# Kernel tuning notes

Measured on AMD Instinct MI355X. Metric: run time of the kernel, lower is better.

## Reference

```python
import jax, jax.numpy as jnp
import numpy as np
from jax import lax

FC = 8      # heads_count
LN_EPS = 1e-5

def _ln(x, g, b):
    mu = jnp.mean(x, axis=-1, keepdims=True)
    var = jnp.mean((x - mu) ** 2, axis=-1, keepdims=True)
    return (x - mu) / jnp.sqrt(var + LN_EPS) * g + b

def _l2norm(x):
    return x / jnp.maximum(jnp.linalg.norm(x, axis=-1, keepdims=True), 1e-12)

def _gelu(x):
    return jax.nn.gelu(x, approximate=False)

def _resize_bilinear(x, oh, ow):
    # x: [N, C, H, W], align_corners=True bilinear (matches F.interpolate)
    h, w = x.shape[2], x.shape[3]
    ys = jnp.linspace(0.0, h - 1.0, oh)
    xs = jnp.linspace(0.0, w - 1.0, ow)
    y0 = jnp.floor(ys).astype(jnp.int32); y1 = jnp.minimum(y0 + 1, h - 1)
    x0 = jnp.floor(xs).astype(jnp.int32); x1 = jnp.minimum(x0 + 1, w - 1)
    dy = (ys - y0).astype(x.dtype)[None, None, :, None]
    dx = (xs - x0).astype(x.dtype)[None, None, None, :]
    rows = x[:, :, y0, :] * (1 - dy) + x[:, :, y1, :] * dy
    return rows[:, :, :, x0] * (1 - dx) + rows[:, :, :, x1] * dx

def _merge_block(x, center, h, w, p):
    # x: [n,l,c], center: [n,s,c]
    n, l, c = x.shape
    hc, wc = h // 2, w // 2
    xn = x.transpose(0, 2, 1).reshape(n, c, h, w)
    cn = center.transpose(0, 2, 1).reshape(n, c, hc, wc)
    up = _resize_bilinear(cn, h, w)
    y = jnp.concatenate([xn, up], axis=1)            # [n,2c,h,w]
    y = y.transpose(0, 2, 3, 1)                      # NHWC
    y = _gelu(y @ p['mb_l0_w'] + p['mb_l0_b'])
    y = y @ p['mb_l1_w'] + p['mb_l1_b']              # [n,h,w,c]
    y = y.transpose(0, 3, 1, 2)                      # NCHW
    mu = jnp.mean(y, axis=(1, 2, 3), keepdims=True)  # GroupNorm(1, c)
    var = jnp.mean((y - mu) ** 2, axis=(1, 2, 3), keepdims=True)
    y = (y - mu) / jnp.sqrt(var + LN_EPS) * p['mb_gn_g'][None, :, None, None] + p['mb_gn_b'][None, :, None, None]
    down = _resize_bilinear(y, hc, wc)
    new_x = y.reshape(n, c, h * w).transpose(0, 2, 1) + x
    new_c = down.reshape(n, c, hc * wc).transpose(0, 2, 1) + center
    return new_x, new_c

def _global_cluster(x0, center1, p):
    n, l, c = x0.shape
    s = center1.shape[1]
    xp = x0 @ p['gc_p0_w'] + p['gc_p0_b']            # [n,l,hd]
    cp = center1 @ p['gc_p1_w'] + p['gc_p1_b']       # [n,s,2hd]
    hd = xp.shape[-1]
    sc = hd // FC
    m = n * FC
    xp = xp.reshape(n, l, FC, sc).transpose(0, 2, 1, 3).reshape(m, l, sc)
    cp = cp.reshape(n, s, FC, 2 * sc).transpose(0, 2, 1, 3).reshape(m, s, 2 * sc)
    cpt, cval = cp[..., :sc], cp[..., sc:]
    sim = jnp.einsum('mlc,msc->mls', _l2norm(xp), _l2norm(cpt))
    sim = jax.nn.sigmoid(p['gc_alpha'] * sim + p['gc_beta'])
    vals = jnp.max(sim, axis=2)                      # [m,l]
    idx = jnp.argmax(sim, axis=2)                    # [m,l]
    disp = vals[..., None] * jnp.take_along_axis(cval, idx[:, :, None], axis=1)  # [m,l,sc]
    disp = disp.reshape(n, FC, l, sc).transpose(0, 2, 1, 3).reshape(n, l, FC * sc)
    return disp @ p['gc_m_w'] + p['gc_m_b']

def _global_block(x0, center1, h, w, p):
    n, l, c = x0.shape
    new = _global_cluster(x0, center1, p)
    new = _ln(new, p['gb_n0_g'], p['gb_n0_b'])
    y = jnp.concatenate([x0, new], axis=2)           # [n,l,2c]
    y = y.reshape(n, h, w, 2 * c)
    y = _gelu(y @ p['gb_lin_w'] + p['gb_lin_b'])     # [n,h,w,2c]
    y = y.transpose(0, 3, 1, 2)                      # NCHW
    y = lax.conv_general_dilated(y, p['gb_conv_w'], (1, 1), ((1, 1), (1, 1)),
                                 dimension_numbers=('NCHW', 'OIHW', 'NCHW'))
    y = y + p['gb_conv_b'][None, :, None, None]
    y = y.reshape(n, c, h * w).transpose(0, 2, 1)    # [n,l,c]
    return _ln(y, p['gb_n1_g'], p['gb_n1_b']) + x0

def setup_inputs() -> dict:
    key = jax.random.key(0)
    ks = jax.random.split(key, 24)
    N, H, W, C, HD = 8, 52, 52, 256, 256
    L = H * W
    S = (H // 2) * (W // 2)
    f32 = jnp.float32
    def xav(k, shape, fin, fout):
        a = (6.0 / (fin + fout)) ** 0.5
        return jax.random.uniform(k, shape, minval=-a, maxval=a, dtype=f32)
    return {
        'x0_16x': jax.random.normal(ks[0], (N, L, C), f32),
        'x1_16x': jax.random.normal(ks[1], (N, L, C), f32),
        'x0_32x': jax.random.normal(ks[2], (N, S, C), f32),
        'x1_32x': jax.random.normal(ks[3], (N, S, C), f32),
        'size0_16x': 52, 'size1_16x': 52,
        'mb_l0_w': xav(ks[4], (2 * C, 2 * C), 2 * C, 2 * C), 'mb_l0_b': jnp.zeros((2 * C,), f32),
        'mb_l1_w': xav(ks[5], (2 * C, C), 2 * C, C), 'mb_l1_b': jnp.zeros((C,), f32),
        'mb_gn_g': jnp.ones((C,), f32), 'mb_gn_b': jnp.zeros((C,), f32),
        'gc_p0_w': xav(ks[6], (C, HD), C, HD), 'gc_p0_b': jnp.zeros((HD,), f32),
        'gc_p1_w': xav(ks[7], (C, 2 * HD), C, 2 * HD), 'gc_p1_b': jnp.zeros((2 * HD,), f32),
        'gc_m_w': xav(ks[8], (HD, C), HD, C), 'gc_m_b': jnp.zeros((C,), f32),
        'gc_alpha': jnp.ones((1,), f32), 'gc_beta': jnp.zeros((1,), f32),
        'gb_n0_g': jnp.ones((C,), f32), 'gb_n0_b': jnp.zeros((C,), f32),
        'gb_lin_w': xav(ks[9], (2 * C, 2 * C), 2 * C, 2 * C), 'gb_lin_b': jnp.zeros((2 * C,), f32),
        'gb_conv_w': xav(ks[10], (C, 2 * C, 3, 3), 2 * C * 9, C * 9), 'gb_conv_b': jnp.zeros((C,), f32),
        'gb_n1_g': jnp.ones((C,), f32), 'gb_n1_b': jnp.zeros((C,), f32),
    }

def reference(x0_16x, x1_16x, x0_32x, x1_32x, size0_16x, size1_16x,
              mb_l0_w, mb_l0_b, mb_l1_w, mb_l1_b, mb_gn_g, mb_gn_b,
              gc_p0_w, gc_p0_b, gc_p1_w, gc_p1_b, gc_m_w, gc_m_b, gc_alpha, gc_beta,
              gb_n0_g, gb_n0_b, gb_lin_w, gb_lin_b, gb_conv_w, gb_conv_b, gb_n1_g, gb_n1_b):
    p = dict(mb_l0_w=mb_l0_w, mb_l0_b=mb_l0_b, mb_l1_w=mb_l1_w, mb_l1_b=mb_l1_b,
             mb_gn_g=mb_gn_g, mb_gn_b=mb_gn_b,
             gc_p0_w=gc_p0_w, gc_p0_b=gc_p0_b, gc_p1_w=gc_p1_w, gc_p1_b=gc_p1_b,
             gc_m_w=gc_m_w, gc_m_b=gc_m_b, gc_alpha=gc_alpha, gc_beta=gc_beta,
             gb_n0_g=gb_n0_g, gb_n0_b=gb_n0_b, gb_lin_w=gb_lin_w, gb_lin_b=gb_lin_b,
             gb_conv_w=gb_conv_w, gb_conv_b=gb_conv_b, gb_n1_g=gb_n1_g, gb_n1_b=gb_n1_b)
    h0 = w0 = int(size0_16x)
    h1 = w1 = int(size1_16x)
    # single layer, type == 'cross' (types=["cross"]); shared weights across streams
    x0_16x, x0_32x = _merge_block(x0_16x, x0_32x, h0, w0, p)
    x1_16x, x1_32x = _merge_block(x1_16x, x1_32x, h1, w1, p)
    x0_16x = _global_block(x0_16x, x1_32x, h0, w0, p)
    x1_16x = _global_block(x1_16x, x0_32x, h1, w1, p)
    return (x0_16x, x1_16x)
```

## Files before the change

### kernel.cpp

```cpp
#include <hip/hip_runtime.h>
#include <math.h>

#define NB 8
#define HH 52
#define WW 52
#define LL 2704
#define CC 256
#define HC 26
#define WC 26
#define SS 676
#define C2 512
#define FCn 8
#define SCn 32
#define M16 (NB*LL)
#define M32 (NB*SS)
#define KCONV (9*C2)
#define SAMP16 ((size_t)LL*CC)
#define SAMP32 ((size_t)SS*CC)

typedef double dvec4 __attribute__((ext_vector_type(4)));
typedef float  f32x4 __attribute__((ext_vector_type(4)));
typedef short  b16x8 __attribute__((ext_vector_type(8)));

__device__ __forceinline__ float  gelu_ct(float x){ return 0.5f*x*(1.0f + erff(x*0.70710678118654752f)); }
__device__ __forceinline__ double gelu_ct(double x){ return 0.5*x*(1.0 + erf(x*0.70710678118654752440)); }

__device__ __forceinline__ short f2b(float x){
    union { float f; unsigned u; } v; v.f = x;
    unsigned r = v.u + 0x7fffu + ((v.u >> 16) & 1u);
    return (short)(r >> 16);
}

template<typename TA0, typename TA1, typename TO, bool GELU, bool CAT>
__global__ __launch_bounds__(256) void gemm_d64(
    const TA0* __restrict__ A0, const TA1* __restrict__ A1, int K0,
    const float* __restrict__ W, const float* __restrict__ Bias,
    TO* __restrict__ Out, int M, int K, int N)
{
    __shared__ double As[16][65];
    __shared__ double Bs[16][65];
    const int t = threadIdx.x;
    const int mBase = blockIdx.y * 64;
    const int nBase = blockIdx.x * 64;
    const int arow = t >> 2;
    const int kof  = (t & 3) << 2;
    const int brow = t >> 4;
    const int nof  = (t & 15) << 2;
    const int w  = t >> 6;
    const int wr = (w >> 1) * 32;
    const int wc = (w & 1) * 32;
    const int lane = t & 63;
    const int lr = lane & 15, lk = lane >> 4;

    dvec4 prm = {0.,0.,0.,0.}, prn = {0.,0.,0.,0.};
    prm = __builtin_amdgcn_mfma_f64_16x16x4f64((double)lr, 0.25, prm, 0,0,0);
    prn = __builtin_amdgcn_mfma_f64_16x16x4f64(0.25, (double)lr, prn, 0,0,0);
    int pm[4], pn[4];
    #pragma unroll
    for (int i=0;i<4;i++){ pm[i] = (int)prm[i]; pn[i] = (int)prn[i]; }

    dvec4 acc00 = {0.,0.,0.,0.}, acc01 = {0.,0.,0.,0.};
    dvec4 acc10 = {0.,0.,0.,0.}, acc11 = {0.,0.,0.,0.};
    const int am = mBase + arow;
    for (int k0 = 0; k0 < K; k0 += 16){
        double a[4] = {0.,0.,0.,0.};
        if (am < M){
            #pragma unroll
            for (int j=0;j<4;j++){
                int k = k0 + kof + j;
                if (!CAT || k < K0) a[j] = (double)A0[(size_t)am*K0 + k];
                else                a[j] = (double)A1[(size_t)am*(K-K0) + (k-K0)];
            }
        }
        double b[4];
        #pragma unroll
        for (int j=0;j<4;j++)
            b[j] = (double)W[(size_t)(k0+brow)*N + nBase + nof + j];
        __syncthreads();
        #pragma unroll
        for (int j=0;j<4;j++) As[kof+j][arow] = a[j];
        #pragma unroll
        for (int j=0;j<4;j++) Bs[brow][nof+j] = b[j];
        __syncthreads();
        #pragma unroll
        for (int ks = 0; ks < 4; ks++){
            double a0 = As[ks*4+lk][wr+lr];
            double a1 = As[ks*4+lk][wr+16+lr];
            double b0 = Bs[ks*4+lk][wc+lr];
            double b1 = Bs[ks*4+lk][wc+16+lr];
            acc00 = __builtin_amdgcn_mfma_f64_16x16x4f64(a0,b0,acc00,0,0,0);
            acc01 = __builtin_amdgcn_mfma_f64_16x16x4f64(a0,b1,acc01,0,0,0);
            acc10 = __builtin_amdgcn_mfma_f64_16x16x4f64(a1,b0,acc10,0,0,0);
            acc11 = __builtin_amdgcn_mfma_f64_16x16x4f64(a1,b1,acc11,0,0,0);
        }
    }
    #pragma unroll
    for (int i=0;i<4;i++){
        const int gm0 = mBase + wr + pm[i];
        const int gm1 = gm0 + 16;
        const int gn0 = nBase + wc + pn[i];
        const int gn1 = gn0 + 16;
        const double bias0 = (double)Bias[gn0];
        const double bias1 = (double)Bias[gn1];
        if (gm0 < M){
            double v0 = acc00[i] + bias0; if (GELU) v0 = gelu_ct(v0);
            double v1 = acc01[i] + bias1; if (GELU) v1 = gelu_ct(v1);
            Out[(size_t)gm0*N + gn0] = (TO)v0;
            Out[(size_t)gm0*N + gn1] = (TO)v1;
        }
        if (gm1 < M){
            double v0 = acc10[i] + bias0; if (GELU) v0 = gelu_ct(v0);
            double v1 = acc11[i] + bias1; if (GELU) v1 = gelu_ct(v1);
            Out[(size_t)gm1*N + gn0] = (TO)v0;
            Out[(size_t)gm1*N + gn1] = (TO)v1;
        }
    }
}

template<bool GELU, bool CAT, bool OUT_BF>
__global__ __launch_bounds__(256) void gemm_bf(
    const short* __restrict__ A0, const short* __restrict__ A1, int K0,
    const short* __restrict__ Wb, const float* __restrict__ Bias,
    void* __restrict__ OutV, int M, int K, int N)
{
    __shared__ short As[64][72];
    __shared__ short Bs[64][72];
    const int t = threadIdx.x;
    const int mBase = blockIdx.y*64, nBase = blockIdx.x*64;
    const int lane = t & 63, lr = lane & 15, lg = lane >> 4;
    const int wr = (t >> 6) * 16;
    const int srow = t >> 2;
    const int sk   = (t & 3) * 16;
    const int am = mBase + srow;
    const int bo = nBase + srow;
    f32x4 acc[4] = {{0,0,0,0},{0,0,0,0},{0,0,0,0},{0,0,0,0}};

    for (int c0 = 0; c0 < K; c0 += 64){
        const int kk = c0 + sk;
        const short* ap;
        if (!CAT || kk < K0) ap = A0 + (size_t)am*K0 + kk;
        else                 ap = A1 + (size_t)am*(K-K0) + (kk - K0);
        b16x8 a0 = *(const b16x8*)ap;
        b16x8 a1 = *(const b16x8*)(ap + 8);
        b16x8 bv0 = *(const b16x8*)&Wb[(size_t)bo*K + kk];
        b16x8 bv1 = *(const b16x8*)&Wb[(size_t)bo*K + kk + 8];
        __syncthreads();
        *(b16x8*)&As[srow][sk]     = a0;
        *(b16x8*)&As[srow][sk + 8] = a1;
        *(b16x8*)&Bs[srow][sk]     = bv0;
        *(b16x8*)&Bs[srow][sk + 8] = bv1;
        __syncthreads();
        #pragma unroll
        for (int kc=0;kc<2;kc++){
            b16x8 a = *(const b16x8*)&As[wr + lr][kc*32 + lg*8];
            #pragma unroll
            for (int cb=0;cb<4;cb++){
                b16x8 b = *(const b16x8*)&Bs[cb*16 + lr][kc*32 + lg*8];
                acc[cb] = __builtin_amdgcn_mfma_f32_16x16x32_bf16(a, b, acc[cb], 0,0,0);
            }
        }
    }
    #pragma unroll
    for (int cb=0;cb<4;cb++){
        int col = nBase + cb*16 + lr;
        float bias = Bias[col];
        #pragma unroll
        for (int i=0;i<4;i++){
            int row = mBase + wr + lg*4 + i;
            float v = acc[cb][i] + bias;
            if (GELU) v = gelu_ct(v);
            if (OUT_BF) ((short*)OutV)[(size_t)row*N + col] = f2b(v);
            else        ((float*)OutV)[(size_t)row*N + col] = v;
        }
    }
}

__global__ __launch_bounds__(256) void conv_bf2(const short* __restrict__ Xb,
    const short* __restrict__ WTb, const float* __restrict__ Bias, float* __restrict__ Out)
{
    __shared__ short As[64][72];
    __shared__ short Bs[256][72];
    const int t = threadIdx.x;
    const int mBase = blockIdx.x*64;
    const int lane = t & 63, lr = lane & 15, lg = lane >> 4;
    const int wr = (t >> 6) * 16;
    const int srow = t >> 2;
    const int sk   = (t & 3) * 16;
    const int am = mBase + srow;
    const int an = am / LL; const int ahw = am % LL;
    const int ah = ahw / WW; const int aw = ahw % WW;
    f32x4 acc[16];
    #pragma unroll
    for (int i=0;i<16;i++) acc[i] = (f32x4){0.f,0.f,0.f,0.f};
    const b16x8 z = {0,0,0,0,0,0,0,0};

    for (int pos = 0; pos < 9; pos++){
        const int dh = pos/3 - 1, dw = pos%3 - 1;
        const int h2 = ah + dh, w2 = aw + dw;
        const bool ok = (h2 >= 0 && h2 < HH && w2 >= 0 && w2 < WW);
        const short* xrow = Xb + ((size_t)(an*LL + h2*WW + w2))*C2;
        for (int c0 = 0; c0 < C2; c0 += 64){
            b16x8 a0 = ok ? *(const b16x8*)&xrow[c0 + sk]     : z;
            b16x8 a1 = ok ? *(const b16x8*)&xrow[c0 + sk + 8] : z;
            b16x8 w0[4], w1[4];
            #pragma unroll
            for (int r=0;r<4;r++){
                const short* wp = WTb + (size_t)(srow + 64*r)*KCONV + pos*C2 + c0 + sk;
                w0[r] = *(const b16x8*)wp;
                w1[r] = *(const b16x8*)(wp + 8);
            }
            __syncthreads();
            *(b16x8*)&As[srow][sk]     = a0;
            *(b16x8*)&As[srow][sk + 8] = a1;
            #pragma unroll
            for (int r=0;r<4;r++){
                *(b16x8*)&Bs[srow + 64*r][sk]     = w0[r];
                *(b16x8*)&Bs[srow + 64*r][sk + 8] = w1[r];
            }
            __syncthreads();
            #pragma unroll
            for (int kc=0;kc<2;kc++){
                b16x8 a = *(const b16x8*)&As[wr + lr][kc*32 + lg*8];
                #pragma unroll
                for (int cb=0;cb<16;cb++){
                    b16x8 b = *(const b16x8*)&Bs[cb*16 + lr][kc*32 + lg*8];
                    acc[cb] = __builtin_amdgcn_mfma_f32_16x16x32_bf16(a, b, acc[cb], 0,0,0);
                }
            }
        }
    }
    #pragma unroll
    for (int cb=0;cb<16;cb++){
        int col = cb*16 + lr;
        float bias = Bias[col];
        #pragma unroll
        for (int i=0;i<4;i++){
            int row = mBase + wr + lg*4 + i;
            Out[(size_t)row*CC + col] = acc[cb][i] + bias;
        }
    }
}

__global__ void wtransb_k(const float* __restrict__ wsrc, short* __restrict__ wt){
    int o = blockIdx.x;
    int i = threadIdx.x;
    #pragma unroll
    for (int pos = 0; pos < 9; pos++)
        wt[(size_t)o*KCONV + pos*C2 + i] = f2b(wsrc[((size_t)o*C2 + i)*9 + pos]);
}

__global__ void wtb_k(const float* __restrict__ src, short* __restrict__ dst, int K, int N){
    int n = blockIdx.x;
    for (int k = threadIdx.x; k < K; k += 256)
        dst[(size_t)n*K + k] = f2b(src[(size_t)k*N + n]);
}

__global__ void d2b_k(const double* __restrict__ src, short* __restrict__ dst){
    int i = blockIdx.x*256 + threadIdx.x;
    dst[i] = f2b((float)src[i]);
}

__global__ void ups_k(const float* __restrict__ cen, double* __restrict__ up){
    int idx = blockIdx.x*256 + threadIdx.x;
    int c = idx & 255;
    int gl = idx >> 8;
    int n = gl / LL, l = gl % LL;
    int h = l / WW, w = l % WW;
    double fy = (h==HH-1) ? (double)(HC-1) : h*((double)(HC-1)/(HH-1));
    double fx = (w==WW-1) ? (double)(WC-1) : w*((double)(WC-1)/(WW-1));
    int y0 = (int)fy; int y1 = min(y0+1, HC-1);
    int x0 = (int)fx; int x1 = min(x0+1, WC-1);
    double dy = fy - y0, dx = fx - x0;
    const float* base = cen + (size_t)n*SAMP32 + c;
    double v00 = (double)base[(size_t)(y0*WC + x0)*CC];
    double v01 = (double)base[(size_t)(y0*WC + x1)*CC];
    double v10 = (double)base[(size_t)(y1*WC + x0)*CC];
    double v11 = (double)base[(size_t)(y1*WC + x1)*CC];
    double r0 = v00*(1.0-dy) + v10*dy;
    double r1 = v01*(1.0-dy) + v11*dy;
    up[idx] = r0*(1.0-dx) + r1*dx;
}

__global__ __launch_bounds__(256) void gn_stats_k(const double* __restrict__ t2c,
    double* __restrict__ stats, int nOff){
    const double* p = t2c + (size_t)blockIdx.y*SAMP16;
    int i0 = blockIdx.x*4096 + threadIdx.x;
    double s = 0.0, q = 0.0;
    #pragma unroll
    for (int r = 0; r < 16; r++){
        double v = p[i0 + r*256];
        s += v; q += v*v;
    }
    #pragma unroll
    for (int off = 32; off; off >>= 1){
        s += __shfl_xor(s, off);
        q += __shfl_xor(q, off);
    }
    __shared__ double ls[4], lq[4];
    int wid = threadIdx.x >> 6;
    if ((threadIdx.x & 63) == 0){ ls[wid] = s; lq[wid] = q; }
    __syncthreads();
    if (threadIdx.x == 0){
        int n = nOff + blockIdx.y;
        atomicAdd(&stats[n*2+0], ls[0]+ls[1]+ls[2]+ls[3]);
        atomicAdd(&stats[n*2+1], lq[0]+lq[1]+lq[2]+lq[3]);
    }
}

__global__ void merge_x_k(const double* __restrict__ t2c, const float* __restrict__ x,
    const float* __restrict__ g, const float* __restrict__ b,
    const double* __restrict__ stats, int nOff, double* __restrict__ mxn){
    int idx = blockIdx.x*256 + threadIdx.x;
    const double inv = 1.0/((double)LL*CC);
    int c = idx & (CC-1);
    int n = nOff + idx / (LL*CC);
    double mu = stats[2*n]*inv;
    double var = stats[2*n+1]*inv - mu*mu;
    double r = 1.0/sqrt(var + 1e-5);
    mxn[idx] = (t2c[idx]-mu)*r*(double)g[c] + (double)b[c] + (double)x[idx];
}

__global__ void merge_c_k(const double* __restrict__ t2c, const float* __restrict__ cen,
    const float* __restrict__ g, const float* __restrict__ b,
    const double* __restrict__ stats, int nOff, double* __restrict__ mcn){
    int idx = blockIdx.x*256 + threadIdx.x;
    int c = idx & 255;
    int ns = idx >> 8;
    int nl = ns / SS, s = ns % SS;
    int i = s / WC, j = s % WC;
    double fy = (i==WC-1) ? (double)(HH-1) : i*((double)(HH-1)/(HC-1));
    double fx = (j==WC-1) ? (double)(WW-1) : j*((double)(WW-1)/(WC-1));
    int y0 = (int)fy; int y1 = min(y0+1, HH-1);
    int x0 = (int)fx; int x1 = min(x0+1, WW-1);
    double dy = fy - y0, dx = fx - x0;
    const double* base = t2c + (size_t)nl*SAMP16 + c;
    double v00 = base[(size_t)(y0*WW + x0)*CC];
    double v01 = base[(size_t)(y0*WW + x1)*CC];
    double v10 = base[(size_t)(y1*WW + x0)*CC];
    double v11 = base[(size_t)(y1*WW + x1)*CC];
    double r0 = v00*(1.0-dy) + v10*dy;
    double r1 = v01*(1.0-dy) + v11*dy;
    double v = r0*(1.0-dx) + r1*dx;
    const double inv = 1.0/((double)LL*CC);
    int n = nOff + nl;
    double mu = stats[2*n]*inv;
    double var = stats[2*n+1]*inv - mu*mu;
    double r = 1.0/sqrt(var + 1e-5);
    mcn[idx] = (v-mu)*r*(double)g[c] + (double)b[c] + (double)cen[idx];
}

__global__ __launch_bounds__(256) void cptn_k(const double* __restrict__ cp, double* __restrict__ ctn){
    int ns = blockIdx.x;
    int n = ns / SS, s = ns % SS;
    int hgrp = threadIdx.x >> 5, k = threadIdx.x & 31;
    double v = cp[(size_t)ns*C2 + hgrp*64 + k];
    double q = v*v;
    #pragma unroll
    for (int off = 16; off; off >>= 1) q += __shfl_xor(q, off, 32);
    double d = fmax(sqrt(q), 1e-12);
    ctn[((size_t)(n*FCn + hgrp)*SS + s)*SCn + k] = v/d;
}

__global__ __launch_bounds__(256) void xnorm_k(const double* __restrict__ xpc, double* __restrict__ xn){
    int t = threadIdx.x;
    int g = t >> 5, k = t & 31;
    int gl = blockIdx.x*8 + g;
    int nl = gl / LL, l = gl % LL;
    int h = blockIdx.y;
    double v = xpc[(size_t)gl*CC + h*SCn + k];
    double q = v*v;
    #pragma unroll
    for (int off = 16; off; off >>= 1) q += __shfl_xor(q, off, 32);
    xn[((size_t)(nl*FCn + h)*LL + l)*SCn + k] = v / fmax(sqrt(q), 1e-12);
}

__global__ __launch_bounds__(256) void sim3_k(
    const double* __restrict__ xn,
    const double* __restrict__ ctn,
    const double* __restrict__ cp,
    const float* __restrict__ alpha_p, const float* __restrict__ beta_p,
    int nOff, short* __restrict__ dispb)
{
    __shared__ double xs[32][65];
    __shared__ double cs[32][65];
    const int t = threadIdx.x;
    const int lBase = blockIdx.x * 64;
    const int h = blockIdx.y;
    const int nl = blockIdx.z;
    const int n = nOff + nl;
    const int w  = t >> 6;
    const int wr = (w >> 1) * 32;
    const int wc = (w & 1) * 32;
    const int lane = t & 63;
    const int lr = lane & 15, lk = lane >> 4;
    const double alpha = (double)alpha_p[0], beta = (double)beta_p[0];

    dvec4 prm = {0.,0.,0.,0.}, prn = {0.,0.,0.,0.};
    prm = __builtin_amdgcn_mfma_f64_16x16x4f64((double)lr, 0.25, prm, 0,0,0);
    prn = __builtin_amdgcn_mfma_f64_16x16x4f64(0.25, (double)lr, prn, 0,0,0);
    int pm[4], pn[4];
    #pragma unroll
    for (int i=0;i<4;i++){ pm[i] = (int)prm[i]; pn[i] = (int)prn[i]; }

    const double* xb = xn + ((size_t)(nl*FCn + h)*LL + lBase)*SCn;
    const int lav = min(64, LL - lBase);
    #pragma unroll
    for (int r = 0; r < 8; r++){
        int idx = t + r*256;
        int li = idx >> 5, ki = idx & 31;
        xs[ki][li] = (li < lav) ? xb[idx] : 0.0;
    }

    double bz[2][2][4];
    int    bs[2][2][4];
    #pragma unroll
    for (int rf=0; rf<2; rf++)
        #pragma unroll
        for (int j=0; j<2; j++)
            #pragma unroll
            for (int i=0; i<4; i++){ bz[rf][j][i] = -1.0e300; bs[rf][j][i] = 0; }

    const double* cbase = ctn + ((size_t)(n*FCn + h))*SS*SCn;
    for (int sBase = 0; sBase < SS; sBase += 64){
        const int sav = min(64, SS - sBase);
        const double* cb = cbase + (size_t)sBase*SCn;
        __syncthreads();
        #pragma unroll
        for (int r = 0; r < 8; r++){
            int idx = t + r*256;
            int si = idx >> 5, ki = idx & 31;
            cs[ki][si] = (si < sav) ? cb[idx] : 0.0;
        }
        __syncthreads();
        dvec4 a00 = {0.,0.,0.,0.}, a01 = {0.,0.,0.,0.};
        dvec4 a10 = {0.,0.,0.,0.}, a11 = {0.,0.,0.,0.};
        #pragma unroll
        for (int ks = 0; ks < 8; ks++){
            double xa0 = xs[ks*4+lk][wr+lr];
            double xa1 = xs[ks*4+lk][wr+16+lr];
            double cb0 = cs[ks*4+lk][wc+lr];
            double cb1 = cs[ks*4+lk][wc+16+lr];
            a00 = __builtin_amdgcn_mfma_f64_16x16x4f64(xa0,cb0,a00,0,0,0);
            a01 = __builtin_amdgcn_mfma_f64_16x16x4f64(xa0,cb1,a01,0,0,0);
            a10 = __builtin_amdgcn_mfma_f64_16x16x4f64(xa1,cb0,a10,0,0,0);
            a11 = __builtin_amdgcn_mfma_f64_16x16x4f64(xa1,cb1,a11,0,0,0);
        }
        #pragma unroll
        for (int i=0;i<4;i++){
            int s0 = sBase + wc + pn[i];
            int s1 = s0 + 16;
            if (s0 < SS){
                double z = alpha*a00[i] + beta;
                if (z > bz[0][0][i]){ bz[0][0][i] = z; bs[0][0][i] = s0; }
                z = alpha*a10[i] + beta;
                if (z > bz[1][0][i]){ bz[1][0][i] = z; bs[1][0][i] = s0; }
            }
            if (s1 < SS){
                double z = alpha*a01[i] + beta;
                if (z > bz[0][1][i]){ bz[0][1][i] = z; bs[0][1][i] = s1; }
                z = alpha*a11[i] + beta;
                if (z > bz[1][1][i]){ bz[1][1][i] = z; bs[1][1][i] = s1; }
            }
        }
    }
    __syncthreads();
    double* redv = &xs[0][0];
    int*    redi = (int*)&cs[0][0];
    #pragma unroll
    for (int rf=0; rf<2; rf++){
        #pragma unroll
        for (int i=0;i<4;i++){
            double z0 = bz[rf][0][i]; int i0 = bs[rf][0][i];
            double z1 = bz[rf][1][i]; int i1 = bs[rf][1][i];
            bool take1 = (z1 > z0) || (z1 == z0 && i1 < i0);
            double z = take1 ? z1 : z0;
            int    s = take1 ? i1 : i0;
            int row = wr + rf*16 + pm[i];
            int cls = (w & 1)*16 + pn[i];
            redv[row*32 + cls] = z;
            redi[row*32 + cls] = s;
        }
    }
    __syncthreads();
    if (t < 64){
        double best = redv[t*32]; int bi = redi[t*32];
        #pragma unroll
        for (int c = 1; c < 32; c++){
            double v = redv[t*32 + c]; int ii = redi[t*32 + c];
            if (v > best || (v == best && ii < bi)){ best = v; bi = ii; }
        }
        int l = lBase + t;
        if (l < LL){
            double val;
            if (best >= 0.0) val = 1.0/(1.0 + exp(-best));
            else { double e = exp(best); val = e/(1.0+e); }
            const double* cv = cp + ((size_t)(n*SS + bi))*C2 + h*64 + 32;
            short* dr = dispb + ((size_t)(n*LL + l))*CC + h*SCn;
            #pragma unroll
            for (int k=0;k<32;k++) dr[k] = f2b((float)(val*cv[k]));
        }
    }
}

__global__ __launch_bounds__(256) void ln_bf_k(const float* __restrict__ y,
    const float* __restrict__ g, const float* __restrict__ b, short* __restrict__ ob){
    int row = blockIdx.x*4 + (threadIdx.x >> 6);
    int lane = threadIdx.x & 63;
    const float* rp = y + (size_t)row*CC;
    float4 v = *(const float4*)(rp + lane*4);
    float s = v.x+v.y+v.z+v.w;
    float q = v.x*v.x+v.y*v.y+v.z*v.z+v.w*v.w;
    #pragma unroll
    for (int off = 32; off; off >>= 1){ s += __shfl_xor(s, off); q += __shfl_xor(q, off); }
    float mu = s*(1.0f/CC);
    float var = q*(1.0f/CC) - mu*mu;
    float r = rsqrtf(var + 1e-5f);
    int c = lane*4;
    float4 gv = *(const float4*)(g+c);
    float4 bv = *(const float4*)(b+c);
    short* op = ob + (size_t)row*CC + c;
    op[0] = f2b((v.x-mu)*r*gv.x+bv.x);
    op[1] = f2b((v.y-mu)*r*gv.y+bv.y);
    op[2] = f2b((v.z-mu)*r*gv.z+bv.z);
    op[3] = f2b((v.w-mu)*r*gv.w+bv.w);
}

__global__ __launch_bounds__(256) void final_k(float* __restrict__ y, const double* __restrict__ res,
    const float* __restrict__ g, const float* __restrict__ b){
    int row = blockIdx.x*4 + (threadIdx.x >> 6);
    int lane = threadIdx.x & 63;
    float* rp = y + (size_t)row*CC;
    const double* xp = res + (size_t)row*CC;
    float4 v = *(const float4*)(rp + lane*4);
    float s = v.x+v.y+v.z+v.w;
    float q = v.x*v.x+v.y*v.y+v.z*v.z+v.w*v.w;
    #pragma unroll
    for (int off = 32; off; off >>= 1){ s += __shfl_xor(s, off); q += __shfl_xor(q, off); }
    float mu = s*(1.0f/CC);
    float var = q*(1.0f/CC) - mu*mu;
    float r = rsqrtf(var + 1e-5f);
    int c = lane*4;
    float4 gv = *(const float4*)(g+c);
    float4 bv = *(const float4*)(b+c);
    float4 o;
    o.x = (v.x-mu)*r*gv.x+bv.x + (float)xp[c+0];
    o.y = (v.y-mu)*r*gv.y+bv.y + (float)xp[c+1];
    o.z = (v.z-mu)*r*gv.z+bv.z + (float)xp[c+2];
    o.w = (v.w-mu)*r*gv.w+bv.w + (float)xp[c+3];
    *(float4*)(rp+c) = o;
}

extern "C" void kernel_launch(void* const* d_in, const int* in_sizes, int n_in,
                              void* d_out, int out_size, void* d_ws, size_t ws_size,
                              hipStream_t stream)
{
    const float* x16[2] = {(const float*)d_in[0], (const float*)d_in[1]};
    const float* x32[2] = {(const float*)d_in[2], (const float*)d_in[3]};
    const float* mb_l0_w = (const float*)d_in[6];
    const float* mb_l0_b = (const float*)d_in[7];
    const float* mb_l1_w = (const float*)d_in[8];
    const float* mb_l1_b = (const float*)d_in[9];
    const float* mb_gn_g = (const float*)d_in[10];
    const float* mb_gn_b = (const float*)d_in[11];
    const float* gc_p0_w = (const float*)d_in[12];
    const float* gc_p0_b = (const float*)d_in[13];
    const float* gc_p1_w = (const float*)d_in[14];
    const float* gc_p1_b = (const float*)d_in[15];
    const float* gc_m_w  = (const float*)d_in[16];
    const float* gc_m_b  = (const float*)d_in[17];
    const float* gc_alpha= (const float*)d_in[18];
    const float* gc_beta = (const float*)d_in[19];
    const float* gb_n0_g = (const float*)d_in[20];
    const float* gb_n0_b = (const float*)d_in[21];
    const float* gb_lin_w= (const float*)d_in[22];
    const float* gb_lin_b= (const float*)d_in[23];
    const float* gb_conv_w=(const float*)d_in[24];
    const float* gb_conv_b=(const float*)d_in[25];
    const float* gb_n1_g = (const float*)d_in[26];
    const float* gb_n1_b = (const float*)d_in[27];

    const size_t F8  = (size_t)M16*CC*8;
    const size_t G8  = (size_t)M32*CC*8;
    const size_t WT4 = (size_t)KCONV*CC*4;

    char* base = (char*)d_ws;
    double* mx[2] = { (double*)base, (double*)(base + F8) };
    double* mc[2] = { (double*)(base + 2*F8), (double*)(base + 2*F8 + G8) };
    char*   pWT   = base + 2*F8 + 2*G8;
    short*  WTb   = (short*)pWT;
    short*  WLb   = (short*)(pWT + 2359296);
    short*  WMb   = (short*)(pWT + 2883584);
    double* stats = (double*)(pWT + WT4);
    char*   E     = pWT + WT4 + 256;
    const size_t base_need = 2*F8 + 2*G8 + WT4 + 256;

    const size_t T2  = (size_t)LL*CC*8;
    const size_t T1  = (size_t)LL*C2*8;
    int nb = 1;
    {
        const int cands[4] = {8,4,2,1};
        for (int ci = 0; ci < 4; ci++){
            int c = cands[ci];
            size_t merge_r  = (size_t)c*(2*T2 + T1);
            size_t global_r = 22151168ull + 11075584ull + (size_t)c*2*T2 + 11075584ull + 11075584ull;
            size_t r = merge_r > global_r ? merge_r : global_r;
            if (base_need + r <= ws_size){ nb = c; break; }
            if (c == 1) return;
        }
    }

    double* t2c = (double*)E;
    double* t1c = (double*)(E + nb*T2);
    double* upc = (double*)(E + nb*(T2 + T1));
    double* cp    = (double*)E;
    double* ctn   = (double*)(E + 22151168);
    double* xpc   = (double*)(E + 33226752);
    double* xn    = (double*)(E + 33226752 + nb*T2);
    short*  dispb = (short*) (E + 33226752 + 2*(size_t)nb*T2);
    short*  mxb   = (short*) (E + 33226752 + 2*(size_t)nb*T2 + 11075584);
    float*  Dbuf  = (float*) E;
    short*  Dbufb = (short*) (E + 22151168);
    short*  Bbufb = (short*) E;

    wtransb_k<<<CC, C2, 0, stream>>>(gb_conv_w, WTb);
    wtb_k<<<C2, 256, 0, stream>>>(gb_lin_w, WLb, C2, C2);
    wtb_k<<<CC, 256, 0, stream>>>(gc_m_w, WMb, CC, CC);

    const int Mc = nb*LL;
    const int mTiles = (Mc + 63) / 64;

    for (int i = 0; i < 2; i++){
        hipMemsetAsync(stats, 0, 16*sizeof(double), stream);
        for (int ch = 0; ch < NB; ch += nb){
            const float* x16c = x16[i] + (size_t)ch*SAMP16;
            const float* x32c = x32[i] + (size_t)ch*SAMP32;
            ups_k<<<nb*LL, 256, 0, stream>>>(x32c, upc);
            gemm_d64<float,double,double,true,true><<<dim3(8, mTiles), 256, 0, stream>>>(
                x16c, upc, CC, mb_l0_w, mb_l0_b, t1c, Mc, C2, C2);
            gemm_d64<double,double,double,false,false><<<dim3(4, mTiles), 256, 0, stream>>>(
                t1c, (const double*)nullptr, C2, mb_l1_w, mb_l1_b, t2c, Mc, C2, CC);
            gn_stats_k<<<dim3(169, nb), 256, 0, stream>>>(t2c, stats, ch);
            merge_x_k<<<nb*LL, 256, 0, stream>>>(t2c, x16c,
                mb_gn_g, mb_gn_b, stats, ch, mx[i] + (size_t)ch*SAMP16);
            merge_c_k<<<nb*SS, 256, 0, stream>>>(t2c, x32c,
                mb_gn_g, mb_gn_b, stats, ch, mc[i] + (size_t)ch*SAMP32);
        }
    }

    float* outp[2] = { (float*)d_out, (float*)d_out + (size_t)M16*CC };
    for (int i = 0; i < 2; i++){
        const double* xi64 = mx[i];
        const double* ci64 = mc[1-i];
        gemm_d64<double,double,double,false,false><<<dim3(8, 85), 256, 0, stream>>>(
            ci64, (const double*)nullptr, CC, gc_p1_w, gc_p1_b, cp, M32, CC, C2);
        cptn_k<<<M32, 256, 0, stream>>>(cp, ctn);
        for (int ch = 0; ch < NB; ch += nb){
            gemm_d64<double,double,double,false,false><<<dim3(4, mTiles), 256, 0, stream>>>(
                xi64 + (size_t)ch*SAMP16, (const double*)nullptr, CC, gc_p0_w, gc_p0_b,
                xpc, Mc, CC, CC);
            xnorm_k<<<dim3(nb*(LL/8), FCn), 256, 0, stream>>>(xpc, xn);
            sim3_k<<<dim3((LL+63)/64, FCn, nb), 256, 0, stream>>>(
                xn, ctn, cp, gc_alpha, gc_beta, ch, dispb);
        }
        d2b_k<<<(M16*CC)/256, 256, 0, stream>>>(xi64, mxb);
        gemm_bf<false,false,false><<<dim3(4, 338), 256, 0, stream>>>(
            dispb, (const short*)nullptr, CC, WMb, gc_m_b, Dbuf, M16, CC, CC);
        ln_bf_k<<<M16/4, 256, 0, stream>>>(Dbuf, gb_n0_g, gb_n0_b, Dbufb);
        gemm_bf<true,true,true><<<dim3(8, 338), 256, 0, stream>>>(
            mxb, Dbufb, CC, WLb, gb_lin_b, Bbufb, M16, C2, C2);
        conv_bf2<<<338, 256, 0, stream>>>(Bbufb, WTb, gb_conv_b, outp[i]);
        final_k<<<M16/4, 256, 0, stream>>>(outp[i], xi64, gb_n1_g, gb_n1_b);
    }
}
```

Measured before the change: 2.570 ms.

## Prefetch fp64 GEMM tiles, shrink conv tile, defer L2 normalization into sim kernel

```diff
diff --git a/kernel.cpp b/kernel.cpp
--- a/kernel.cpp
+++ b/kernel.cpp
@@ -37,14 +37,14 @@
     const float* __restrict__ W, const float* __restrict__ Bias,
     TO* __restrict__ Out, int M, int K, int N)
 {
-    __shared__ double As[16][65];
-    __shared__ double Bs[16][65];
+    __shared__ double As[32][65];
+    __shared__ double Bs[32][65];
     const int t = threadIdx.x;
     const int mBase = blockIdx.y * 64;
     const int nBase = blockIdx.x * 64;
     const int arow = t >> 2;
-    const int kof  = (t & 3) << 2;
-    const int brow = t >> 4;
+    const int kofA = (t & 3) << 3;
+    const int kb   = (t >> 4) << 1;
     const int nof  = (t & 15) << 2;
     const int w  = t >> 6;
     const int wr = (w >> 1) * 32;
@@ -62,28 +62,40 @@
     dvec4 acc00 = {0.,0.,0.,0.}, acc01 = {0.,0.,0.,0.};
     dvec4 acc10 = {0.,0.,0.,0.}, acc11 = {0.,0.,0.,0.};
     const int am = mBase + arow;
-    for (int k0 = 0; k0 < K; k0 += 16){
-        double a[4] = {0.,0.,0.,0.};
-        if (am < M){
-            #pragma unroll
-            for (int j=0;j<4;j++){
-                int k = k0 + kof + j;
-                if (!CAT || k < K0) a[j] = (double)A0[(size_t)am*K0 + k];
-                else                a[j] = (double)A1[(size_t)am*(K-K0) + (k-K0)];
+
+    double aReg[8], bReg[8];
+    auto loadA = [&](int k0){
+        #pragma unroll
+        for (int j=0;j<8;j++){
+            int k = k0 + kofA + j;
+            double v = 0.0;
+            if (am < M){
+                if (!CAT || k < K0) v = (double)A0[(size_t)am*K0 + k];
+                else                v = (double)A1[(size_t)am*(K-K0) + (k-K0)];
             }
-        }
-        double b[4];
-        #pragma unroll
-        for (int j=0;j<4;j++)
-            b[j] = (double)W[(size_t)(k0+brow)*N + nBase + nof + j];
+            aReg[j] = v;
+        }
+    };
+    auto loadB = [&](int k0){
+        #pragma unroll
+        for (int r=0;r<2;r++)
+            #pragma unroll
+            for (int j=0;j<4;j++)
+                bReg[r*4+j] = (double)W[(size_t)(k0+kb+r)*N + nBase + nof + j];
+    };
+    loadA(0); loadB(0);
+    for (int k0 = 0; k0 < K; k0 += 32){
         __syncthreads();
         #pragma unroll
-        for (int j=0;j<4;j++) As[kof+j][arow] = a[j];
-        #pragma unroll
-        for (int j=0;j<4;j++) Bs[brow][nof+j] = b[j];
+        for (int j=0;j<8;j++) As[kofA+j][arow] = aReg[j];
+        #pragma unroll
+        for (int r=0;r<2;r++)
+            #pragma unroll
+            for (int j=0;j<4;j++) Bs[kb+r][nof+j] = bReg[r*4+j];
         __syncthreads();
-        #pragma unroll
-        for (int ks = 0; ks < 4; ks++){
+        if (k0 + 32 < K){ loadA(k0+32); loadB(k0+32); }
+        #pragma unroll
+        for (int ks = 0; ks < 8; ks++){
             double a0 = As[ks*4+lk][wr+lr];
             double a1 = As[ks*4+lk][wr+16+lr];
             double b0 = Bs[ks*4+lk][wc+lr];
@@ -178,20 +190,24 @@
 __global__ __launch_bounds__(256) void conv_bf2(const short* __restrict__ Xb,
     const short* __restrict__ WTb, const float* __restrict__ Bias, float* __restrict__ Out)
 {
-    __shared__ short As[64][72];
+    __shared__ short As[32][72];
     __shared__ short Bs[256][72];
     const int t = threadIdx.x;
-    const int mBase = blockIdx.x*64;
+    const int mBase = blockIdx.x*32;
     const int lane = t & 63, lr = lane & 15, lg = lane >> 4;
-    const int wr = (t >> 6) * 16;
+    const int w = t >> 6;
+    const int wr16 = (w & 1) * 16;
+    const int ch   = (w >> 1) * 8;
+    const int arow = t >> 3;
+    const int ska  = (t & 7) * 8;
     const int srow = t >> 2;
     const int sk   = (t & 3) * 16;
-    const int am = mBase + srow;
+    const int am = mBase + arow;
     const int an = am / LL; const int ahw = am % LL;
     const int ah = ahw / WW; const int aw = ahw % WW;
-    f32x4 acc[16];
-    #pragma unroll
-    for (int i=0;i<16;i++) acc[i] = (f32x4){0.f,0.f,0.f,0.f};
+    f32x4 acc[8];
+    #pragma unroll
+    for (int i=0;i<8;i++) acc[i] = (f32x4){0.f,0.f,0.f,0.f};
     const b16x8 z = {0,0,0,0,0,0,0,0};
 
     for (int pos = 0; pos < 9; pos++){
@@ -200,8 +216,7 @@
         const bool ok = (h2 >= 0 && h2 < HH && w2 >= 0 && w2 < WW);
         const short* xrow = Xb + ((size_t)(an*LL + h2*WW + w2))*C2;
         for (int c0 = 0; c0 < C2; c0 += 64){
-            b16x8 a0 = ok ? *(const b16x8*)&xrow[c0 + sk]     : z;
-            b16x8 a1 = ok ? *(const b16x8*)&xrow[c0 + sk + 8] : z;
+            b16x8 a0 = ok ? *(const b16x8*)&xrow[c0 + ska] : z;
             b16x8 w0[4], w1[4];
             #pragma unroll
             for (int r=0;r<4;r++){
@@ -210,8 +225,7 @@
                 w1[r] = *(const b16x8*)(wp + 8);
             }
             __syncthreads();
-            *(b16x8*)&As[srow][sk]     = a0;
-            *(b16x8*)&As[srow][sk + 8] = a1;
+            *(b16x8*)&As[arow][ska] = a0;
             #pragma unroll
             for (int r=0;r<4;r++){
                 *(b16x8*)&Bs[srow + 64*r][sk]     = w0[r];
@@ -220,22 +234,22 @@
             __syncthreads();
             #pragma unroll
             for (int kc=0;kc<2;kc++){
-                b16x8 a = *(const b16x8*)&As[wr + lr][kc*32 + lg*8];
+                b16x8 a = *(const b16x8*)&As[wr16 + lr][kc*32 + lg*8];
                 #pragma unroll
-                for (int cb=0;cb<16;cb++){
-                    b16x8 b = *(const b16x8*)&Bs[cb*16 + lr][kc*32 + lg*8];
+                for (int cb=0;cb<8;cb++){
+                    b16x8 b = *(const b16x8*)&Bs[(ch+cb)*16 + lr][kc*32 + lg*8];
                     acc[cb] = __builtin_amdgcn_mfma_f32_16x16x32_bf16(a, b, acc[cb], 0,0,0);
                 }
             }
         }
     }
     #pragma unroll
-    for (int cb=0;cb<16;cb++){
-        int col = cb*16 + lr;
+    for (int cb=0;cb<8;cb++){
+        int col = (ch+cb)*16 + lr;
         float bias = Bias[col];
         #pragma unroll
         for (int i=0;i<4;i++){
-            int row = mBase + wr + lg*4 + i;
+            int row = mBase + wr16 + lg*4 + i;
             Out[(size_t)row*CC + col] = acc[cb][i] + bias;
         }
     }
@@ -361,7 +375,7 @@
     ctn[((size_t)(n*FCn + hgrp)*SS + s)*SCn + k] = v/d;
 }
 
-__global__ __launch_bounds__(256) void xnorm_k(const double* __restrict__ xpc, double* __restrict__ xn){
+__global__ __launch_bounds__(256) void norm_k(const double* __restrict__ xpc, double* __restrict__ norms){
     int t = threadIdx.x;
     int g = t >> 5, k = t & 31;
     int gl = blockIdx.x*8 + g;
@@ -371,11 +385,12 @@
     double q = v*v;
     #pragma unroll
     for (int off = 16; off; off >>= 1) q += __shfl_xor(q, off, 32);
-    xn[((size_t)(nl*FCn + h)*LL + l)*SCn + k] = v / fmax(sqrt(q), 1e-12);
+    if (k == 0) norms[((size_t)nl*FCn + h)*LL + l] = fmax(sqrt(q), 1e-12);
 }
 
 __global__ __launch_bounds__(256) void sim3_k(
-    const double* __restrict__ xn,
+    const double* __restrict__ xpc,
+    const double* __restrict__ norms,
     const double* __restrict__ ctn,
     const double* __restrict__ cp,
     const float* __restrict__ alpha_p, const float* __restrict__ beta_p,
@@ -394,6 +409,7 @@
     const int lane = t & 63;
     const int lr = lane & 15, lk = lane >> 4;
     const double alpha = (double)alpha_p[0], beta = (double)beta_p[0];
+    const double sgn = (alpha >= 0.0) ? 1.0 : -1.0;
 
     dvec4 prm = {0.,0.,0.,0.}, prn = {0.,0.,0.,0.};
     prm = __builtin_amdgcn_mfma_f64_16x16x4f64((double)lr, 0.25, prm, 0,0,0);
@@ -402,13 +418,14 @@
     #pragma unroll
     for (int i=0;i<4;i++){ pm[i] = (int)prm[i]; pn[i] = (int)prn[i]; }
 
-    const double* xb = xn + ((size_t)(nl*FCn + h)*LL + lBase)*SCn;
     const int lav = min(64, LL - lBase);
     #pragma unroll
     for (int r = 0; r < 8; r++){
         int idx = t + r*256;
         int li = idx >> 5, ki = idx & 31;
-        xs[ki][li] = (li < lav) ? xb[idx] : 0.0;
+        double v = 0.0;
+        if (li < lav) v = xpc[((size_t)nl*LL + lBase + li)*CC + h*SCn + ki];
+        xs[ki][li] = v;
     }
 
     double bz[2][2][4];
@@ -450,15 +467,15 @@
             int s0 = sBase + wc + pn[i];
             int s1 = s0 + 16;
             if (s0 < SS){
-                double z = alpha*a00[i] + beta;
+                double z = sgn*a00[i];
                 if (z > bz[0][0][i]){ bz[0][0][i] = z; bs[0][0][i] = s0; }
-                z = alpha*a10[i] + beta;
+                z = sgn*a10[i];
                 if (z > bz[1][0][i]){ bz[1][0][i] = z; bs[1][0][i] = s0; }
             }
             if (s1 < SS){
-                double z = alpha*a01[i] + beta;
+                double z = sgn*a01[i];
                 if (z > bz[0][1][i]){ bz[0][1][i] = z; bs[0][1][i] = s1; }
-                z = alpha*a11[i] + beta;
+                z = sgn*a11[i];
                 if (z > bz[1][1][i]){ bz[1][1][i] = z; bs[1][1][i] = s1; }
             }
         }
@@ -491,9 +508,11 @@
         }
         int l = lBase + t;
         if (l < LL){
+            double nrm = norms[((size_t)nl*FCn + h)*LL + l];
+            double zb = alpha*((sgn*best)/nrm) + beta;
             double val;
-            if (best >= 0.0) val = 1.0/(1.0 + exp(-best));
-            else { double e = exp(best); val = e/(1.0+e); }
+            if (zb >= 0.0) val = 1.0/(1.0 + exp(-zb));
+            else { double e = exp(zb); val = e/(1.0+e); }
             const double* cv = cp + ((size_t)(n*SS + bi))*C2 + h*64 + 32;
             short* dr = dispb + ((size_t)(n*LL + l))*CC + h*SCn;
             #pragma unroll
@@ -596,13 +615,14 @@
 
     const size_t T2  = (size_t)LL*CC*8;
     const size_t T1  = (size_t)LL*C2*8;
+    const size_t TN  = (size_t)FCn*LL*8;
     int nb = 1;
     {
         const int cands[4] = {8,4,2,1};
         for (int ci = 0; ci < 4; ci++){
             int c = cands[ci];
             size_t merge_r  = (size_t)c*(2*T2 + T1);
-            size_t global_r = 22151168ull + 11075584ull + (size_t)c*2*T2 + 11075584ull + 11075584ull;
+            size_t global_r = 22151168ull + 11075584ull + (size_t)c*(T2 + TN) + 11075584ull + 11075584ull;
             size_t r = merge_r > global_r ? merge_r : global_r;
             if (base_need + r <= ws_size){ nb = c; break; }
             if (c == 1) return;
@@ -615,9 +635,9 @@
     double* cp    = (double*)E;
     double* ctn   = (double*)(E + 22151168);
     double* xpc   = (double*)(E + 33226752);
-    double* xn    = (double*)(E + 33226752 + nb*T2);
-    short*  dispb = (short*) (E + 33226752 + 2*(size_t)nb*T2);
-    short*  mxb   = (short*) (E + 33226752 + 2*(size_t)nb*T2 + 11075584);
+    double* norms = (double*)(E + 33226752 + nb*T2);
+    short*  dispb = (short*) (E + 33226752 + (size_t)nb*(T2 + TN));
+    short*  mxb   = (short*) (E + 33226752 + (size_t)nb*(T2 + TN) + 11075584);
     float*  Dbuf  = (float*) E;
     short*  Dbufb = (short*) (E + 22151168);
     short*  Bbufb = (short*) E;
@@ -658,9 +678,9 @@
             gemm_d64<double,double,double,false,false><<<dim3(4, mTiles), 256, 0, stream>>>(
                 xi64 + (size_t)ch*SAMP16, (const double*)nullptr, CC, gc_p0_w, gc_p0_b,
                 xpc, Mc, CC, CC);
-            xnorm_k<<<dim3(nb*(LL/8), FCn), 256, 0, stream>>>(xpc, xn);
+            norm_k<<<dim3(nb*(LL/8), FCn), 256, 0, stream>>>(xpc, norms);
             sim3_k<<<dim3((LL+63)/64, FCn, nb), 256, 0, stream>>>(
-                xn, ctn, cp, gc_alpha, gc_beta, ch, dispb);
+                xpc, norms, ctn, cp, gc_alpha, gc_beta, ch, dispb);
         }
         d2b_k<<<(M16*CC)/256, 256, 0, stream>>>(xi64, mxb);
         gemm_bf<false,false,false><<<dim3(4, 338), 256, 0, stream>>>(
@@ -668,7 +688,7 @@
         ln_bf_k<<<M16/4, 256, 0, stream>>>(Dbuf, gb_n0_g, gb_n0_b, Dbufb);
         gemm_bf<true,true,true><<<dim3(8, 338), 256, 0, stream>>>(
             mxb, Dbufb, CC, WLb, gb_lin_b, Bbufb, M16, C2, C2);
-        conv_bf2<<<338, 256, 0, stream>>>(Bbufb, WTb, gb_conv_b, outp[i]);
+        conv_bf2<<<M16/32, 256, 0, stream>>>(Bbufb, WTb, gb_conv_b, outp[i]);
         final_k<<<M16/4, 256, 0, stream>>>(outp[i], xi64, gb_n1_g, gb_n1_b);
     }
 }
```

New measurement: 2.383 ms. 1.08x faster.
